# Optimization experiments

Hardware: AMD Instinct MI355X
Metric: run time of the kernel (lower is better)

The kernel has to match this reference:

```python
import jax, jax.numpy as jnp
import numpy as np
import math

MAX_REL_POS = 32  # max_relative_position

def _sincos_table(d_model, max_len):
    pos = np.arange(max_len)[:, None].astype(np.float32)
    div = np.exp(np.arange(0, d_model, 2).astype(np.float32) * (-math.log(10000.0) / d_model))
    pe = np.zeros((max_len, d_model), dtype=np.float32)
    pe[:, 0::2] = np.sin(pos * div)
    pe[:, 1::2] = np.cos(pos * div)
    return jnp.asarray(pe)

def setup_inputs() -> dict:
    rng = jax.random.key(0)
    k1, k2, k3 = jax.random.split(rng, 3)
    B, H, S, D = 4, 16, 1024, 64
    pe = _sincos_table(D, 2 * MAX_REL_POS + 1)  # fixed (non-trainable) buffer
    return {
        "query": jax.random.normal(k1, (B, H, S, D), jnp.float32),
        "key": jax.random.normal(k2, (B, H, S, D), jnp.float32),
        "value": jax.random.normal(k3, (B, H, S, D), jnp.float32),
        "pe_k": pe,
        "pe_v": pe,
    }

def reference(query, key, value, pe_k, pe_v):
    B, H, S, D = query.shape
    # relative distance indices: clip(k - q, -P, P) + P  -> [S, S]
    dist = jnp.clip(jnp.arange(S)[None, :] - jnp.arange(S)[:, None],
                    -MAX_REL_POS, MAX_REL_POS) + MAX_REL_POS
    R_k = pe_k[dist]  # [S, S, D]
    R_v = pe_v[dist]  # [S, S, D]
    scores = jnp.einsum('bhqd,bhkd->bhqk', query, key)
    scores = scores + jnp.einsum('bhqd,qkd->bhqk', query, R_k)
    scores = scores / math.sqrt(D)
    # one_direction=True -> causal mask
    causal = jnp.tril(jnp.ones((S, S), dtype=bool))
    scores = jnp.where(causal[None, None], scores, jnp.float32(-1e9))
    p_attn = jax.nn.softmax(scores, axis=-1)
    output = jnp.einsum('bhqk,bhkd->bhqd', p_attn, value)
    output = output + jnp.einsum('bhqv,qvd->bhqd', p_attn, R_v)
    return output, p_attn
```

## Files before the change

kernel.cpp:

```cpp
#include <hip/hip_runtime.h>

typedef __attribute__((ext_vector_type(8))) short bfrag;
typedef __attribute__((ext_vector_type(4))) float ffrag;

namespace {
constexpr int Sc = 1024, Dc = 64;
constexpr int P2 = 72;
constexpr int PQ = 64;
constexpr int PW = 33;
constexpr float SCALE = 0.125f;
}

__device__ __forceinline__ unsigned short f2bf(float f) {
    unsigned u = __builtin_bit_cast(unsigned, f);
    u += 0x7fffu + ((u >> 16) & 1u);
    return (unsigned short)(u >> 16);
}
__device__ __forceinline__ bfrag pack8(float4 a, float4 b) {
    bfrag r;
    r[0] = (short)f2bf(a.x); r[1] = (short)f2bf(a.y);
    r[2] = (short)f2bf(a.z); r[3] = (short)f2bf(a.w);
    r[4] = (short)f2bf(b.x); r[5] = (short)f2bf(b.y);
    r[6] = (short)f2bf(b.z); r[7] = (short)f2bf(b.w);
    return r;
}
#define MFMA(a, b, c) __builtin_amdgcn_mfma_f32_16x16x32_bf16((a), (b), (c), 0, 0, 0)

#define BAR()                                             \
    do {                                                  \
        asm volatile("s_waitcnt lgkmcnt(0)" ::: "memory");\
        __builtin_amdgcn_s_barrier();                     \
    } while (0)

__global__ __launch_bounds__(256, 2)
void relattn(const float* __restrict__ Qg, const float* __restrict__ Kg,
             const float* __restrict__ Vg, const float* __restrict__ pek,
             const float* __restrict__ pev, float* __restrict__ outg,
             float* __restrict__ pbuf)
{
    __shared__ __align__(16) char smem[72448];
    unsigned short* Ks0 = (unsigned short*)smem;
    unsigned short* Ks1 = (unsigned short*)(smem + 9216);
    unsigned short* Vt0 = (unsigned short*)(smem + 18432);
    unsigned short* Vt1 = (unsigned short*)(smem + 27648);
    unsigned short* Pt0 = (unsigned short*)(smem + 36864);
    unsigned short* Pt1 = (unsigned short*)(smem + 46080);
    float* Ts = (float*)(smem + 55296);
    unsigned short* Qs = (unsigned short*)(smem + 63744);
    float* Ws = (float*)(smem + 63744);
    float* W0 = (float*)(smem + 72192);
    float* Ot = (float*)smem;

    const int tid  = threadIdx.x;
    const int bh   = blockIdx.y;
    const int wv   = tid >> 6;
    const int lane = tid & 63;
    const int n    = lane & 15;
    const int quad = lane >> 4;

    const float* Qbh = Qg + (size_t)bh * Sc * Dc;
    const float* Kbh = Kg + (size_t)bh * Sc * Dc;
    const float* Vbh = Vg + (size_t)bh * Sc * Dc;
    float* pbh = pbuf + (size_t)bh * Sc * Sc;
    float* obh = outg + (size_t)bh * Sc * Dc;

    const int sr  = tid >> 2;
    const int sc4 = (tid & 3) * 16;
    const int kp  = tid & 31;
    const int vd0 = (tid >> 5) * 8;

    const int rr = tid >> 4;
    const int c4 = tid & 15;

    for (int half = 0; half < 2; ++half) {
        const int qt = half ? (15 - (int)blockIdx.x) : (int)blockIdx.x;
        const int qrow = wv * 16 + quad * 4;

        BAR();

        float4 k0a, k0b, k0c, k0d;
        {
            const float* ksrc = Kbh + (size_t)sr * Dc + sc4;
            k0a = *(const float4*)(ksrc);
            k0b = *(const float4*)(ksrc + 4);
            k0c = *(const float4*)(ksrc + 8);
            k0d = *(const float4*)(ksrc + 12);
        }
        {
            const float* src = Qbh + (size_t)(qt * 64 + sr) * Dc + sc4;
            float4 a = *(const float4*)(src);
            float4 b = *(const float4*)(src + 4);
            float4 c = *(const float4*)(src + 8);
            float4 d = *(const float4*)(src + 12);
            *(bfrag*)&Qs[sr * PQ + sc4]     = pack8(a, b);
            *(bfrag*)&Qs[sr * PQ + sc4 + 8] = pack8(c, d);
        }
        for (int i = tid; i < 135; i += 256) {
            bfrag z = {};
            *(bfrag*)&Ks0[33 * P2 + i * 8] = z;
        }
        if (tid < 132) {
            int r = tid >> 2, c0 = (tid & 3) * 16;
            const float* src = pek + (size_t)r * Dc + c0;
            float4 a = *(const float4*)(src);
            float4 b = *(const float4*)(src + 4);
            float4 c = *(const float4*)(src + 8);
            float4 d = *(const float4*)(src + 12);
            *(bfrag*)&Ks0[r * P2 + c0]     = pack8(a, b);
            *(bfrag*)&Ks0[r * P2 + c0 + 8] = pack8(c, d);
        }
        BAR();

        bfrag qa0 = *(bfrag*)&Qs[(wv * 16 + n) * PQ + quad * 8];
        bfrag qa1 = *(bfrag*)&Qs[(wv * 16 + n) * PQ + 32 + quad * 8];

        #pragma unroll
        for (int sub = 0; sub < 3; ++sub) {
            bfrag b0 = *(bfrag*)&Ks0[(sub * 16 + n) * P2 + quad * 8];
            bfrag b1 = *(bfrag*)&Ks0[(sub * 16 + n) * P2 + 32 + quad * 8];
            ffrag c = {};
            c = MFMA(qa0, b0, c);
            c = MFMA(qa1, b1, c);
            int j = sub * 16 + n;
            if (j <= 32) {
                #pragma unroll
                for (int reg = 0; reg < 4; ++reg)
                    Ts[(qrow + reg) * PW + j] = c[reg];
            }
        }
        *(bfrag*)&Ks1[sr * P2 + sc4]     = pack8(k0a, k0b);
        *(bfrag*)&Ks1[sr * P2 + sc4 + 8] = pack8(k0c, k0d);
        float4 pka, pkb, pkc, pkd;
        if (qt >= 1) {
            const float* ksrc = Kbh + (size_t)(64 + sr) * Dc + sc4;
            pka = *(const float4*)(ksrc);
            pkb = *(const float4*)(ksrc + 4);
            pkc = *(const float4*)(ksrc + 8);
            pkd = *(const float4*)(ksrc + 12);
        }
        BAR();

        float ts0[4];
        #pragma unroll
        for (int reg = 0; reg < 4; ++reg) ts0[reg] = Ts[(qrow + reg) * PW];

        for (int idx = tid; idx < 64 * PW; idx += 256) Ws[idx] = 0.f;

        {
            const int zb = (qt + 1) * 64;
            if (zb < Sc) {
                const int z4 = (Sc - zb) >> 2;
                const float4 z = make_float4(0.f, 0.f, 0.f, 0.f);
                for (int r = 0; r < 64; ++r) {
                    float4* rp = (float4*)(pbh + (size_t)(qt * 64 + r) * Sc + zb);
                    for (int cz = tid; cz < z4; cz += 256) rp[cz] = z;
                }
            }
        }

        float lsum[4] = {0.f, 0.f, 0.f, 0.f};
        for (int kt = 0; kt <= qt; ++kt) {
            const bool bnd = (kt >= qt - 1);
            unsigned short* Kc = (kt & 1) ? Ks0 : Ks1;
            unsigned short* Kn = (kt & 1) ? Ks1 : Ks0;
            #pragma unroll
            for (int sub = 0; sub < 4; ++sub) {
                bfrag b0 = *(bfrag*)&Kc[(sub * 16 + n) * P2 + quad * 8];
                bfrag b1 = *(bfrag*)&Kc[(sub * 16 + n) * P2 + 32 + quad * 8];
                ffrag c = {};
                c = MFMA(qa0, b0, c);
                c = MFMA(qa1, b1, c);
                const int k = kt * 64 + sub * 16 + n;
                if (!bnd) {
                    #pragma unroll
                    for (int reg = 0; reg < 4; ++reg)
                        lsum[reg] += __expf((c[reg] + ts0[reg]) * SCALE);
                } else {
                    #pragma unroll
                    for (int reg = 0; reg < 4; ++reg) {
                        int jrel = k - (qt * 64 + qrow + reg) + 32;
                        if (jrel <= 32) {
                            int jcl = jrel < 0 ? 0 : jrel;
                            lsum[reg] += __expf((c[reg] + Ts[(qrow + reg) * PW + jcl]) * SCALE);
                        }
                    }
                }
            }
            if (kt < qt) {
                *(bfrag*)&Kn[sr * P2 + sc4]     = pack8(pka, pkb);
                *(bfrag*)&Kn[sr * P2 + sc4 + 8] = pack8(pkc, pkd);
            }
            if (kt + 2 <= qt) {
                const float* ksrc = Kbh + (size_t)((kt + 2) * 64 + sr) * Dc + sc4;
                pka = *(const float4*)(ksrc);
                pkb = *(const float4*)(ksrc + 4);
                pkc = *(const float4*)(ksrc + 8);
                pkd = *(const float4*)(ksrc + 12);
            }
            BAR();
        }
        float rinv[4];
        #pragma unroll
        for (int reg = 0; reg < 4; ++reg) {
            float l = lsum[reg];
            l += __shfl_xor(l, 1);
            l += __shfl_xor(l, 2);
            l += __shfl_xor(l, 4);
            l += __shfl_xor(l, 8);
            rinv[reg] = 1.f / l;
        }

        {
            const float* ksrc = Kbh + (size_t)sr * Dc + sc4;
            float4 a = *(const float4*)(ksrc);
            float4 b = *(const float4*)(ksrc + 4);
            float4 c = *(const float4*)(ksrc + 8);
            float4 d = *(const float4*)(ksrc + 12);
            *(bfrag*)&Ks0[sr * P2 + sc4]     = pack8(a, b);
            *(bfrag*)&Ks0[sr * P2 + sc4 + 8] = pack8(c, d);
        }
        if (qt >= 1) {
            const float* ksrc = Kbh + (size_t)(64 + sr) * Dc + sc4;
            pka = *(const float4*)(ksrc);
            pkb = *(const float4*)(ksrc + 4);
            pkc = *(const float4*)(ksrc + 8);
            pkd = *(const float4*)(ksrc + 12);
        }
        float4 pva, pvb, pvc, pvd;
        {
            const float* vsrc = Vbh + (size_t)(2 * kp) * Dc + vd0;
            pva = *(const float4*)(vsrc);
            pvb = *(const float4*)(vsrc + 4);
            pvc = *(const float4*)(vsrc + Dc);
            pvd = *(const float4*)(vsrc + Dc + 4);
        }
        BAR();

        ffrag oacc[4];
        #pragma unroll
        for (int i = 0; i < 4; ++i) { ffrag z = {}; oacc[i] = z; }

        for (int kt = 0; kt <= qt; ++kt) {
            const bool bnd = (kt >= qt - 1);
            unsigned short* Kc  = (kt & 1) ? Ks1 : Ks0;
            unsigned short* Kn  = (kt & 1) ? Ks0 : Ks1;
            unsigned short* Vc  = (kt & 1) ? Vt1 : Vt0;
            unsigned short* Vp  = (kt & 1) ? Vt0 : Vt1;
            unsigned short* Ptc = (kt & 1) ? Pt1 : Pt0;
            unsigned short* Ptp = (kt & 1) ? Pt0 : Pt1;

            #pragma unroll
            for (int sub = 0; sub < 4; ++sub) {
                bfrag b0 = *(bfrag*)&Kc[(sub * 16 + n) * P2 + quad * 8];
                bfrag b1 = *(bfrag*)&Kc[(sub * 16 + n) * P2 + 32 + quad * 8];
                ffrag c = {};
                c = MFMA(qa0, b0, c);
                c = MFMA(qa1, b1, c);
                const int k = kt * 64 + sub * 16 + n;
                if (!bnd) {
                    #pragma unroll
                    for (int reg = 0; reg < 4; ++reg) {
                        float p = __expf((c[reg] + ts0[reg]) * SCALE) * rinv[reg];
                        Ptc[(qrow + reg) * P2 + sub * 16 + n] = (unsigned short)f2bf(p);
                    }
                } else {
                    #pragma unroll
                    for (int reg = 0; reg < 4; ++reg) {
                        int jrel = k - (qt * 64 + qrow + reg) + 32;
                        float p = 0.f;
                        if (jrel <= 32) {
                            int jcl = jrel < 0 ? 0 : jrel;
                            p = __expf((c[reg] + Ts[(qrow + reg) * PW + jcl]) * SCALE) * rinv[reg];
                        }
                        Ptc[(qrow + reg) * P2 + sub * 16 + n] = (unsigned short)f2bf(p);
                        if ((unsigned)(jrel - 1) < 32u) Ws[(qrow + reg) * PW + jrel - 1] = p;
                    }
                }
            }
            if (kt < qt) {
                *(bfrag*)&Kn[sr * P2 + sc4]     = pack8(pka, pkb);
                *(bfrag*)&Kn[sr * P2 + sc4 + 8] = pack8(pkc, pkd);
            }
            {
                float r0[8] = {pva.x, pva.y, pva.z, pva.w, pvb.x, pvb.y, pvb.z, pvb.w};
                float r1[8] = {pvc.x, pvc.y, pvc.z, pvc.w, pvd.x, pvd.y, pvd.z, pvd.w};
                #pragma unroll
                for (int i = 0; i < 8; ++i) {
                    unsigned pk = (unsigned)f2bf(r0[i]) | ((unsigned)f2bf(r1[i]) << 16);
                    *(unsigned*)&Vc[(vd0 + i) * P2 + 2 * kp] = pk;
                }
            }
            if (kt + 2 <= qt) {
                const float* ksrc = Kbh + (size_t)((kt + 2) * 64 + sr) * Dc + sc4;
                pka = *(const float4*)(ksrc);
                pkb = *(const float4*)(ksrc + 4);
                pkc = *(const float4*)(ksrc + 8);
                pkd = *(const float4*)(ksrc + 12);
            }
            if (kt + 1 <= qt) {
                const float* vsrc = Vbh + (size_t)((kt + 1) * 64 + 2 * kp) * Dc + vd0;
                pva = *(const float4*)(vsrc);
                pvb = *(const float4*)(vsrc + 4);
                pvc = *(const float4*)(vsrc + Dc);
                pvd = *(const float4*)(vsrc + Dc + 4);
            }
            if (kt >= 1) {
                bfrag pb0 = *(bfrag*)&Ptp[(wv * 16 + n) * P2 + quad * 8];
                bfrag pb1 = *(bfrag*)&Ptp[(wv * 16 + n) * P2 + 32 + quad * 8];
                #pragma unroll
                for (int ds = 0; ds < 4; ++ds) {
                    bfrag va0 = *(bfrag*)&Vp[(ds * 16 + n) * P2 + quad * 8];
                    bfrag va1 = *(bfrag*)&Vp[(ds * 16 + n) * P2 + 32 + quad * 8];
                    oacc[ds] = MFMA(va0, pb0, oacc[ds]);
                    oacc[ds] = MFMA(va1, pb1, oacc[ds]);
                }
                float* base = pbh + ((size_t)(qt * 64 + rr) * Sc + (kt - 1) * 64 + c4 * 4);
                #pragma unroll
                for (int step = 0; step < 4; ++step) {
                    const int r = step * 16 + rr;
                    const unsigned short* ps = &Ptp[r * P2 + c4 * 4];
                    unsigned two0 = *(const unsigned*)(ps);
                    unsigned two1 = *(const unsigned*)(ps + 2);
                    float4 v;
                    v.x = __builtin_bit_cast(float, (two0 & 0xffffu) << 16);
                    v.y = __builtin_bit_cast(float, two0 & 0xffff0000u);
                    v.z = __builtin_bit_cast(float, (two1 & 0xffffu) << 16);
                    v.w = __builtin_bit_cast(float, two1 & 0xffff0000u);
                    *(float4*)(base + (size_t)(step * 16) * Sc) = v;
                }
            }
            BAR();
        }
        {
            unsigned short* Ptp = (qt & 1) ? Pt1 : Pt0;
            unsigned short* Vp  = (qt & 1) ? Vt1 : Vt0;
            bfrag pb0 = *(bfrag*)&Ptp[(wv * 16 + n) * P2 + quad * 8];
            bfrag pb1 = *(bfrag*)&Ptp[(wv * 16 + n) * P2 + 32 + quad * 8];
            #pragma unroll
            for (int ds = 0; ds < 4; ++ds) {
                bfrag va0 = *(bfrag*)&Vp[(ds * 16 + n) * P2 + quad * 8];
                bfrag va1 = *(bfrag*)&Vp[(ds * 16 + n) * P2 + 32 + quad * 8];
                oacc[ds] = MFMA(va0, pb0, oacc[ds]);
                oacc[ds] = MFMA(va1, pb1, oacc[ds]);
            }
            float* base = pbh + ((size_t)(qt * 64 + rr) * Sc + qt * 64 + c4 * 4);
            #pragma unroll
            for (int step = 0; step < 4; ++step) {
                const int r = step * 16 + rr;
                const unsigned short* ps = &Ptp[r * P2 + c4 * 4];
                unsigned two0 = *(const unsigned*)(ps);
                unsigned two1 = *(const unsigned*)(ps + 2);
                float4 v;
                v.x = __builtin_bit_cast(float, (two0 & 0xffffu) << 16);
                v.y = __builtin_bit_cast(float, two0 & 0xffff0000u);
                v.z = __builtin_bit_cast(float, (two1 & 0xffffu) << 16);
                v.w = __builtin_bit_cast(float, two1 & 0xffff0000u);
                *(float4*)(base + (size_t)(step * 16) * Sc) = v;
            }
        }
        BAR();

        if (tid < 64) {
            float s = 0.f;
            #pragma unroll
            for (int j = 0; j < 32; ++j) s += Ws[tid * PW + j];
            W0[tid] = 1.f - s;
        }
        {
            int q = tid >> 2, j0 = (tid & 3) * 8;
            #pragma unroll
            for (int i = 0; i < 8; i += 2) {
                unsigned pk = (unsigned)f2bf(Ws[q * PW + j0 + i]) |
                              ((unsigned)f2bf(Ws[q * PW + j0 + i + 1]) << 16);
                *(unsigned*)&Pt0[q * P2 + j0 + i] = pk;
            }
        }
        {
            int jj = tid >> 3, d0 = (tid & 7) * 8;
            const float* src = pev + (size_t)(jj + 1) * Dc + d0;
            float4 a = *(const float4*)(src);
            float4 b = *(const float4*)(src + 4);
            float vr[8] = {a.x, a.y, a.z, a.w, b.x, b.y, b.z, b.w};
            #pragma unroll
            for (int i = 0; i < 8; ++i)
                Vt0[(d0 + i) * P2 + jj] = (unsigned short)f2bf(vr[i]);
        }
        BAR();
        {
            bfrag pb = *(bfrag*)&Pt0[(wv * 16 + n) * P2 + quad * 8];
            #pragma unroll
            for (int ds = 0; ds < 4; ++ds) {
                bfrag va = *(bfrag*)&Vt0[(ds * 16 + n) * P2 + quad * 8];
                oacc[ds] = MFMA(va, pb, oacc[ds]);
            }
        }
        float w0q = W0[wv * 16 + n];
        #pragma unroll
        for (int ds = 0; ds < 4; ++ds) {
            float4 ov;
            ov.x = oacc[ds][0] + w0q * pev[ds * 16 + quad * 4 + 0];
            ov.y = oacc[ds][1] + w0q * pev[ds * 16 + quad * 4 + 1];
            ov.z = oacc[ds][2] + w0q * pev[ds * 16 + quad * 4 + 2];
            ov.w = oacc[ds][3] + w0q * pev[ds * 16 + quad * 4 + 3];
            *(float4*)&Ot[(wv * 16 + n) * 68 + ds * 16 + quad * 4] = ov;
        }
        BAR();
        {
            int r = tid >> 2, c0 = (tid & 3) * 16;
            float* dst = obh + (size_t)(qt * 64 + r) * Dc + c0;
            *(float4*)(dst)      = *(float4*)&Ot[r * 68 + c0];
            *(float4*)(dst + 4)  = *(float4*)&Ot[r * 68 + c0 + 4];
            *(float4*)(dst + 8)  = *(float4*)&Ot[r * 68 + c0 + 8];
            *(float4*)(dst + 12) = *(float4*)&Ot[r * 68 + c0 + 12];
        }
    }
}

extern "C" void kernel_launch(void* const* d_in, const int* in_sizes, int n_in,
                              void* d_out, int out_size, void* d_ws, size_t ws_size,
                              hipStream_t stream)
{
    const float* Q   = (const float*)d_in[0];
    const float* K   = (const float*)d_in[1];
    const float* V   = (const float*)d_in[2];
    const float* pek = (const float*)d_in[3];
    const float* pev = (const float*)d_in[4];
    float* out  = (float*)d_out;
    float* pbuf = out + (size_t)64 * Sc * Dc;

    dim3 grid(8, 64);
    relattn<<<grid, 256, 0, stream>>>(Q, K, V, pek, pev, out, pbuf);
}
```

Baseline: 375.4 us.

## Split softmax row-sum pass and upper-triangle zeroing into a separate parallel kernel

Moves the first pass over keys, which computes softmax denominators, out of the main kernel into a new kernel launched per (q-tile, k-tile) pair that combines partial sums with atomicAdd into a workspace. That new kernel also zeroes the masked upper-triangle tiles of the probability output. The main kernel then reads the reciprocal row sums and runs only the second pass. The aim is to spread the serial per-block first pass over many more workgroups and take the zeroing stores off the main kernel. The cost is an extra memset and kernel launch, reloading Q and pe per tile, atomics, and summation order that now varies between runs.

```diff
diff --git a/kernel.cpp b/kernel.cpp
--- a/kernel.cpp
+++ b/kernel.cpp
@@ -32,11 +32,138 @@
         __builtin_amdgcn_s_barrier();                     \
     } while (0)
 
+__global__ __launch_bounds__(256, 4)
+void lsum_zero(const float* __restrict__ Qg, const float* __restrict__ Kg,
+               const float* __restrict__ pek, float* __restrict__ pbuf,
+               float* __restrict__ lws)
+{
+    const int qt = (int)blockIdx.x >> 4;
+    const int kt = (int)blockIdx.x & 15;
+    const int bh = blockIdx.y;
+    const int tid = threadIdx.x;
+    float* pbh = pbuf + (size_t)bh * Sc * Sc;
+
+    if (kt > qt) {
+        const int rr = tid >> 4, c4 = tid & 15;
+        const float4 z = make_float4(0.f, 0.f, 0.f, 0.f);
+        float* base = pbh + (size_t)(qt * 64 + rr) * Sc + kt * 64 + c4 * 4;
+        #pragma unroll
+        for (int s = 0; s < 4; ++s)
+            *(float4*)(base + (size_t)(s * 16) * Sc) = z;
+        return;
+    }
+
+    __shared__ __align__(16) char sm[32768];
+    unsigned short* Qs = (unsigned short*)sm;
+    unsigned short* Ks = (unsigned short*)(sm + 8192);
+    unsigned short* Ps = (unsigned short*)(sm + 17408);
+    float* Ts = (float*)(sm + 24320);
+
+    const int wv = tid >> 6, lane = tid & 63, n = lane & 15, quad = lane >> 4;
+    const int qrow = wv * 16 + quad * 4;
+    const int sr = tid >> 2, sc4 = (tid & 3) * 16;
+    const float* Qbh = Qg + (size_t)bh * Sc * Dc;
+    const float* Kbh = Kg + (size_t)bh * Sc * Dc;
+
+    {
+        const float* src = Qbh + (size_t)(qt * 64 + sr) * Dc + sc4;
+        float4 a = *(const float4*)(src);
+        float4 b = *(const float4*)(src + 4);
+        float4 c = *(const float4*)(src + 8);
+        float4 d = *(const float4*)(src + 12);
+        *(bfrag*)&Qs[sr * PQ + sc4]     = pack8(a, b);
+        *(bfrag*)&Qs[sr * PQ + sc4 + 8] = pack8(c, d);
+    }
+    {
+        const float* src = Kbh + (size_t)(kt * 64 + sr) * Dc + sc4;
+        float4 a = *(const float4*)(src);
+        float4 b = *(const float4*)(src + 4);
+        float4 c = *(const float4*)(src + 8);
+        float4 d = *(const float4*)(src + 12);
+        *(bfrag*)&Ks[sr * P2 + sc4]     = pack8(a, b);
+        *(bfrag*)&Ks[sr * P2 + sc4 + 8] = pack8(c, d);
+    }
+    if (tid < 135) {
+        bfrag z = {};
+        *(bfrag*)&Ps[33 * P2 + tid * 8] = z;
+    }
+    if (tid < 132) {
+        int r = tid >> 2, c0 = (tid & 3) * 16;
+        const float* src = pek + (size_t)r * Dc + c0;
+        float4 a = *(const float4*)(src);
+        float4 b = *(const float4*)(src + 4);
+        float4 c = *(const float4*)(src + 8);
+        float4 d = *(const float4*)(src + 12);
+        *(bfrag*)&Ps[r * P2 + c0]     = pack8(a, b);
+        *(bfrag*)&Ps[r * P2 + c0 + 8] = pack8(c, d);
+    }
+    __syncthreads();
+
+    bfrag qa0 = *(bfrag*)&Qs[(wv * 16 + n) * PQ + quad * 8];
+    bfrag qa1 = *(bfrag*)&Qs[(wv * 16 + n) * PQ + 32 + quad * 8];
+
+    #pragma unroll
+    for (int sub = 0; sub < 3; ++sub) {
+        bfrag b0 = *(bfrag*)&Ps[(sub * 16 + n) * P2 + quad * 8];
+        bfrag b1 = *(bfrag*)&Ps[(sub * 16 + n) * P2 + 32 + quad * 8];
+        ffrag c = {};
+        c = MFMA(qa0, b0, c);
+        c = MFMA(qa1, b1, c);
+        int j = sub * 16 + n;
+        if (j <= 32) {
+            #pragma unroll
+            for (int reg = 0; reg < 4; ++reg)
+                Ts[(qrow + reg) * PW + j] = c[reg];
+        }
+    }
+    __syncthreads();
+
+    float ts0[4];
+    #pragma unroll
+    for (int reg = 0; reg < 4; ++reg) ts0[reg] = Ts[(qrow + reg) * PW];
+
+    const bool bnd = (kt >= qt - 1);
+    float ls[4] = {0.f, 0.f, 0.f, 0.f};
+    #pragma unroll
+    for (int sub = 0; sub < 4; ++sub) {
+        bfrag b0 = *(bfrag*)&Ks[(sub * 16 + n) * P2 + quad * 8];
+        bfrag b1 = *(bfrag*)&Ks[(sub * 16 + n) * P2 + 32 + quad * 8];
+        ffrag c = {};
+        c = MFMA(qa0, b0, c);
+        c = MFMA(qa1, b1, c);
+        const int k = kt * 64 + sub * 16 + n;
+        if (!bnd) {
+            #pragma unroll
+            for (int reg = 0; reg < 4; ++reg)
+                ls[reg] += __expf((c[reg] + ts0[reg]) * SCALE);
+        } else {
+            #pragma unroll
+            for (int reg = 0; reg < 4; ++reg) {
+                int jrel = k - (qt * 64 + qrow + reg) + 32;
+                if (jrel <= 32) {
+                    int jcl = jrel < 0 ? 0 : jrel;
+                    ls[reg] += __expf((c[reg] + Ts[(qrow + reg) * PW + jcl]) * SCALE);
+                }
+            }
+        }
+    }
+    #pragma unroll
+    for (int reg = 0; reg < 4; ++reg) {
+        float l = ls[reg];
+        l += __shfl_xor(l, 1);
+        l += __shfl_xor(l, 2);
+        l += __shfl_xor(l, 4);
+        l += __shfl_xor(l, 8);
+        if (n == 0)
+            atomicAdd(&lws[(size_t)bh * Sc + qt * 64 + qrow + reg], l);
+    }
+}
+
 __global__ __launch_bounds__(256, 2)
 void relattn(const float* __restrict__ Qg, const float* __restrict__ Kg,
              const float* __restrict__ Vg, const float* __restrict__ pek,
              const float* __restrict__ pev, float* __restrict__ outg,
-             float* __restrict__ pbuf)
+             float* __restrict__ pbuf, const float* __restrict__ lws)
 {
     __shared__ __align__(16) char smem[72448];
     unsigned short* Ks0 = (unsigned short*)smem;
@@ -78,6 +205,11 @@
 
         BAR();
 
+        float rinv[4];
+        #pragma unroll
+        for (int reg = 0; reg < 4; ++reg)
+            rinv[reg] = 1.f / lws[(size_t)bh * Sc + qt * 64 + qrow + reg];
+
         float4 k0a, k0b, k0c, k0d;
         {
             const float* ksrc = Kbh + (size_t)sr * Dc + sc4;
@@ -97,7 +229,7 @@
         }
         for (int i = tid; i < 135; i += 256) {
             bfrag z = {};
-            *(bfrag*)&Ks0[33 * P2 + i * 8] = z;
+            *(bfrag*)&Ks1[33 * P2 + i * 8] = z;
         }
         if (tid < 132) {
             int r = tid >> 2, c0 = (tid & 3) * 16;
@@ -106,8 +238,8 @@
             float4 b = *(const float4*)(src + 4);
             float4 c = *(const float4*)(src + 8);
             float4 d = *(const float4*)(src + 12);
-            *(bfrag*)&Ks0[r * P2 + c0]     = pack8(a, b);
-            *(bfrag*)&Ks0[r * P2 + c0 + 8] = pack8(c, d);
+            *(bfrag*)&Ks1[r * P2 + c0]     = pack8(a, b);
+            *(bfrag*)&Ks1[r * P2 + c0 + 8] = pack8(c, d);
         }
         BAR();
 
@@ -116,8 +248,8 @@
 
         #pragma unroll
         for (int sub = 0; sub < 3; ++sub) {
-            bfrag b0 = *(bfrag*)&Ks0[(sub * 16 + n) * P2 + quad * 8];
-            bfrag b1 = *(bfrag*)&Ks0[(sub * 16 + n) * P2 + 32 + quad * 8];
+            bfrag b0 = *(bfrag*)&Ks1[(sub * 16 + n) * P2 + quad * 8];
+            bfrag b1 = *(bfrag*)&Ks1[(sub * 16 + n) * P2 + 32 + quad * 8];
             ffrag c = {};
             c = MFMA(qa0, b0, c);
             c = MFMA(qa1, b1, c);
@@ -128,8 +260,8 @@
                     Ts[(qrow + reg) * PW + j] = c[reg];
             }
         }
-        *(bfrag*)&Ks1[sr * P2 + sc4]     = pack8(k0a, k0b);
-        *(bfrag*)&Ks1[sr * P2 + sc4 + 8] = pack8(k0c, k0d);
+        *(bfrag*)&Ks0[sr * P2 + sc4]     = pack8(k0a, k0b);
+        *(bfrag*)&Ks0[sr * P2 + sc4 + 8] = pack8(k0c, k0d);
         float4 pka, pkb, pkc, pkd;
         if (qt >= 1) {
             const float* ksrc = Kbh + (size_t)(64 + sr) * Dc + sc4;
@@ -138,94 +270,6 @@
             pkc = *(const float4*)(ksrc + 8);
             pkd = *(const float4*)(ksrc + 12);
         }
-        BAR();
-
-        float ts0[4];
-        #pragma unroll
-        for (int reg = 0; reg < 4; ++reg) ts0[reg] = Ts[(qrow + reg) * PW];
-
-        for (int idx = tid; idx < 64 * PW; idx += 256) Ws[idx] = 0.f;
-
-        {
-            const int zb = (qt + 1) * 64;
-            if (zb < Sc) {
-                const int z4 = (Sc - zb) >> 2;
-                const float4 z = make_float4(0.f, 0.f, 0.f, 0.f);
-                for (int r = 0; r < 64; ++r) {
-                    float4* rp = (float4*)(pbh + (size_t)(qt * 64 + r) * Sc + zb);
-                    for (int cz = tid; cz < z4; cz += 256) rp[cz] = z;
-                }
-            }
-        }
-
-        float lsum[4] = {0.f, 0.f, 0.f, 0.f};
-        for (int kt = 0; kt <= qt; ++kt) {
-            const bool bnd = (kt >= qt - 1);
-            unsigned short* Kc = (kt & 1) ? Ks0 : Ks1;
-            unsigned short* Kn = (kt & 1) ? Ks1 : Ks0;
-            #pragma unroll
-            for (int sub = 0; sub < 4; ++sub) {
-                bfrag b0 = *(bfrag*)&Kc[(sub * 16 + n) * P2 + quad * 8];
-                bfrag b1 = *(bfrag*)&Kc[(sub * 16 + n) * P2 + 32 + quad * 8];
-                ffrag c = {};
-                c = MFMA(qa0, b0, c);
-                c = MFMA(qa1, b1, c);
-                const int k = kt * 64 + sub * 16 + n;
-                if (!bnd) {
-                    #pragma unroll
-                    for (int reg = 0; reg < 4; ++reg)
-                        lsum[reg] += __expf((c[reg] + ts0[reg]) * SCALE);
-                } else {
-                    #pragma unroll
-                    for (int reg = 0; reg < 4; ++reg) {
-                        int jrel = k - (qt * 64 + qrow + reg) + 32;
-                        if (jrel <= 32) {
-                            int jcl = jrel < 0 ? 0 : jrel;
-                            lsum[reg] += __expf((c[reg] + Ts[(qrow + reg) * PW + jcl]) * SCALE);
-                        }
-                    }
-                }
-            }
-            if (kt < qt) {
-                *(bfrag*)&Kn[sr * P2 + sc4]     = pack8(pka, pkb);
-                *(bfrag*)&Kn[sr * P2 + sc4 + 8] = pack8(pkc, pkd);
-            }
-            if (kt + 2 <= qt) {
-                const float* ksrc = Kbh + (size_t)((kt + 2) * 64 + sr) * Dc + sc4;
-                pka = *(const float4*)(ksrc);
-                pkb = *(const float4*)(ksrc + 4);
-                pkc = *(const float4*)(ksrc + 8);
-                pkd = *(const float4*)(ksrc + 12);
-            }
-            BAR();
-        }
-        float rinv[4];
-        #pragma unroll
-        for (int reg = 0; reg < 4; ++reg) {
-            float l = lsum[reg];
-            l += __shfl_xor(l, 1);
-            l += __shfl_xor(l, 2);
-            l += __shfl_xor(l, 4);
-            l += __shfl_xor(l, 8);
-            rinv[reg] = 1.f / l;
-        }
-
-        {
-            const float* ksrc = Kbh + (size_t)sr * Dc + sc4;
-            float4 a = *(const float4*)(ksrc);
-            float4 b = *(const float4*)(ksrc + 4);
-            float4 c = *(const float4*)(ksrc + 8);
-            float4 d = *(const float4*)(ksrc + 12);
-            *(bfrag*)&Ks0[sr * P2 + sc4]     = pack8(a, b);
-            *(bfrag*)&Ks0[sr * P2 + sc4 + 8] = pack8(c, d);
-        }
-        if (qt >= 1) {
-            const float* ksrc = Kbh + (size_t)(64 + sr) * Dc + sc4;
-            pka = *(const float4*)(ksrc);
-            pkb = *(const float4*)(ksrc + 4);
-            pkc = *(const float4*)(ksrc + 8);
-            pkd = *(const float4*)(ksrc + 12);
-        }
         float4 pva, pvb, pvc, pvd;
         {
             const float* vsrc = Vbh + (size_t)(2 * kp) * Dc + vd0;
@@ -234,6 +278,13 @@
             pvc = *(const float4*)(vsrc + Dc);
             pvd = *(const float4*)(vsrc + Dc + 4);
         }
+        BAR();
+
+        float ts0[4];
+        #pragma unroll
+        for (int reg = 0; reg < 4; ++reg) ts0[reg] = Ts[(qrow + reg) * PW];
+
+        for (int idx = tid; idx < 64 * PW; idx += 256) Ws[idx] = 0.f;
         BAR();
 
         ffrag oacc[4];
@@ -427,7 +478,9 @@
     const float* pev = (const float*)d_in[4];
     float* out  = (float*)d_out;
     float* pbuf = out + (size_t)64 * Sc * Dc;
-
-    dim3 grid(8, 64);
-    relattn<<<grid, 256, 0, stream>>>(Q, K, V, pek, pev, out, pbuf);
-}
+    float* lws  = (float*)d_ws;
+
+    hipMemsetAsync(d_ws, 0, (size_t)64 * Sc * sizeof(float), stream);
+    lsum_zero<<<dim3(256, 64), 256, 0, stream>>>(Q, K, pek, pbuf, lws);
+    relattn<<<dim3(8, 64), 256, 0, stream>>>(Q, K, V, pek, pev, out, pbuf, lws);
+}
```

After: 419.9 us. +11.9%, slower.
